# Optimization experiments

Measured on AMD Instinct MI355X. Metric: run time of the kernel, lower is better.

Reference implementation:

```python
import jax, jax.numpy as jnp
import numpy as np

B_SZ, CH, H, W = 32, 256, 28, 28
D_INNER, D_STATE, D_CONV, DT_RANK, DEPTH = 512, 16, 4, 16, 2


def setup_inputs() -> dict:
    key = jax.random.key(0)
    ks = jax.random.split(key, 10)
    s = 0.02
    A = jnp.broadcast_to(jnp.arange(1, D_STATE + 1, dtype=jnp.float32), (DEPTH, D_INNER, D_STATE))
    return {
        "bbox_feats": jax.random.normal(ks[0], (B_SZ, CH, H, W), jnp.float32),
        "norm_w": jnp.ones((DEPTH, CH), jnp.float32),
        "norm_b": jnp.zeros((DEPTH, CH), jnp.float32),
        "in_proj_w": jax.random.normal(ks[1], (DEPTH, 2 * D_INNER, CH), jnp.float32) * s,
        "conv_w": jax.random.normal(ks[2], (DEPTH, D_INNER, D_CONV), jnp.float32) * 0.1,
        "conv_b": jnp.zeros((DEPTH, D_INNER), jnp.float32),
        "x_proj_w": jax.random.normal(ks[3], (DEPTH, DT_RANK + 2 * D_STATE, D_INNER), jnp.float32) * s,
        "dt_proj_w": jax.random.normal(ks[4], (DEPTH, D_INNER, DT_RANK), jnp.float32) * 0.1,
        "dt_proj_b": jax.random.normal(ks[5], (DEPTH, D_INNER), jnp.float32) * 0.1,
        "A_log": jnp.log(A),
        "D_param": jnp.ones((DEPTH, D_INNER), jnp.float32),
        "out_proj_w": jax.random.normal(ks[6], (DEPTH, CH, D_INNER), jnp.float32) * s,
    }


def _layernorm(x, w, b, eps=1e-5):
    mu = jnp.mean(x, axis=-1, keepdims=True)
    var = jnp.mean(jnp.square(x - mu), axis=-1, keepdims=True)
    return (x - mu) * jax.lax.rsqrt(var + eps) * w + b


def _mamba(x, in_w, cw, cb, xp_w, dtp_w, dtp_b, A_log, Dp, out_w):
    # x: [B, L, d_model]
    B, L, _ = x.shape
    xz = jnp.einsum('bld,ed->ble', x, in_w)          # [B, L, 2*d_inner]
    xi, z = jnp.split(xz, 2, axis=-1)                # each [B, L, d_inner]
    # depthwise causal conv1d (kernel D_CONV, left pad D_CONV-1)
    xpad = jnp.pad(xi, ((0, 0), (D_CONV - 1, 0), (0, 0)))
    xc = cb
    for k in range(D_CONV):
        xc = xc + xpad[:, k:k + L, :] * cw[:, k]
    xc = jax.nn.silu(xc)                             # [B, L, d_inner]
    x_dbl = jnp.einsum('bld,ed->ble', xc, xp_w)      # [B, L, dt_rank+2*d_state]
    dt_r = x_dbl[..., :DT_RANK]
    Bm = x_dbl[..., DT_RANK:DT_RANK + D_STATE]
    Cm = x_dbl[..., DT_RANK + D_STATE:]
    dt = jax.nn.softplus(jnp.einsum('blr,dr->bld', dt_r, dtp_w) + dtp_b)  # [B, L, d_inner]
    A = -jnp.exp(A_log)                              # [d_inner, d_state]

    def step(h, inp):
        dt_t, B_t, C_t, x_t = inp                    # [B,d_inner],[B,d_state],[B,d_state],[B,d_inner]
        dA = jnp.exp(dt_t[:, :, None] * A)           # [B, d_inner, d_state]
        h = h * dA + dt_t[:, :, None] * B_t[:, None, :] * x_t[:, :, None]
        y = jnp.einsum('bds,bs->bd', h, C_t)
        return h, y

    h0 = jnp.zeros((B, D_INNER, D_STATE), x.dtype)
    inputs = (jnp.swapaxes(dt, 0, 1), jnp.swapaxes(Bm, 0, 1),
              jnp.swapaxes(Cm, 0, 1), jnp.swapaxes(xc, 0, 1))
    _, ys = jax.lax.scan(step, h0, inputs)
    y = jnp.swapaxes(ys, 0, 1) + xc * Dp             # [B, L, d_inner]
    y = y * jax.nn.silu(z)
    return jnp.einsum('bld,ed->ble', y, out_w)       # [B, L, d_model]


def reference(bbox_feats, norm_w, norm_b, in_proj_w, conv_w, conv_b,
              x_proj_w, dt_proj_w, dt_proj_b, A_log, D_param, out_proj_w):
    B, C, h, w = bbox_feats.shape
    x = bbox_feats
    for i in range(DEPTH):
        xf = jnp.swapaxes(x.reshape(B, C, h * w), -1, -2)   # [B, L, C]
        xn = _layernorm(xf, norm_w[i], norm_b[i])
        ym = _mamba(xn, in_proj_w[i], conv_w[i], conv_b[i], x_proj_w[i],
                    dt_proj_w[i], dt_proj_b[i], A_log[i], D_param[i], out_proj_w[i])
        x = jnp.swapaxes(ym, -1, -2).reshape(B, C, h, w)
    return x
```

## Files before the change

### kernel.cpp

```cpp
#include <hip/hip_runtime.h>
#include <cstdint>
#include <cstddef>

#define BSZ  32
#define CHN  256
#define LSEQ 784
#define DI   512
#define NCH  16

#define PK_TILE  16384
#define PK_NT    7
#define PK_PERB  (PK_NT * PK_TILE)

typedef unsigned short u16;
typedef short s16x8 __attribute__((ext_vector_type(8)));
typedef float f32x4 __attribute__((ext_vector_type(4)));

__device__ __forceinline__ float b2f(u16 u) {
  union { unsigned int i; float f; } v; v.i = ((unsigned int)u) << 16; return v.f;
}
__device__ __forceinline__ u16 f2b(float f) {
  union { float f; unsigned int i; } v; v.f = f;
  unsigned int x = v.i;
  return (u16)((x + 0x7FFFu + ((x >> 16) & 1u)) >> 16);
}

#define SA_HALF(dv, xv, Q0, Q1, Q2, Q3) do {                                  \
  float dx_ = (dv) * (xv);                                                    \
  float w1_ = __expf(-(dv));                                                  \
  float e2_ = w1_*w1_, e4_ = e2_*e2_, e8_ = e4_*e4_;                          \
  float p3_ = e2_*w1_, p5_ = e4_*w1_, p6_ = e4_*e2_, p7_ = p6_*w1_;           \
  float p9_ = e8_*w1_, p10_ = e8_*e2_, p11_ = p10_*w1_, p12_ = e8_*e4_;       \
  float p13_ = p12_*w1_, p14_ = p12_*e2_, p15_ = p14_*w1_, p16_ = e8_*e8_;    \
  h[0]  = h[0]*w1_  + dx_*Q0.x;  h[1]  = h[1]*e2_  + dx_*Q0.y;                \
  h[2]  = h[2]*p3_  + dx_*Q0.z;  h[3]  = h[3]*e4_  + dx_*Q0.w;                \
  h[4]  = h[4]*p5_  + dx_*Q1.x;  h[5]  = h[5]*p6_  + dx_*Q1.y;                \
  h[6]  = h[6]*p7_  + dx_*Q1.z;  h[7]  = h[7]*e8_  + dx_*Q1.w;                \
  h[8]  = h[8]*p9_  + dx_*Q2.x;  h[9]  = h[9]*p10_ + dx_*Q2.y;                \
  h[10] = h[10]*p11_+ dx_*Q2.z;  h[11] = h[11]*p12_+ dx_*Q2.w;                \
  h[12] = h[12]*p13_+ dx_*Q3.x;  h[13] = h[13]*p14_+ dx_*Q3.y;                \
  h[14] = h[14]*p15_+ dx_*Q3.z;  h[15] = h[15]*p16_+ dx_*Q3.w;                \
} while (0)

#define SC_HALF(dv, xv, zv, Q0, Q1, Q2, Q3, R0, R1, R2, R3, YB) do {          \
  SA_HALF(dv, xv, Q0, Q1, Q2, Q3);                                            \
  float ya_ = h[0]*R0.x;  ya_ = fmaf(h[1], R0.y, ya_);                        \
  ya_ = fmaf(h[2], R0.z, ya_);  ya_ = fmaf(h[3], R0.w, ya_);                  \
  float yb_ = h[4]*R1.x;  yb_ = fmaf(h[5], R1.y, yb_);                        \
  yb_ = fmaf(h[6], R1.z, yb_);  yb_ = fmaf(h[7], R1.w, yb_);                  \
  float yc_ = h[8]*R2.x;  yc_ = fmaf(h[9], R2.y, yc_);                        \
  yc_ = fmaf(h[10], R2.z, yc_); yc_ = fmaf(h[11], R2.w, yc_);                 \
  float yd_ = h[12]*R3.x; yd_ = fmaf(h[13], R3.y, yd_);                       \
  yd_ = fmaf(h[14], R3.z, yd_); yd_ = fmaf(h[15], R3.w, yd_);                 \
  float yy_ = (ya_ + yb_) + (yc_ + yd_) + (xv) * dpar;                        \
  float sg_ = (zv) / (1.f + __expf(-(zv)));                                   \
  YB = f2b(yy_ * sg_);                                                        \
} while (0)

__global__ void k_flag(const unsigned* __restrict__ nwraw, int* __restrict__ flag) {
  if (threadIdx.x == 0 && blockIdx.x == 0) {
    flag[0] = (nwraw[0] == 0x3F803F80u) ? 1 : 0;
    flag[1] = 1;
  }
}

struct CanonSrcs { const void* p[11]; };

__global__ __launch_bounds__(256) void k_canon_all(CanonSrcs s,
                                                   u16* __restrict__ ws,
                                                   const int* __restrict__ flag) {
  const int ns[11]  = {512, 512, 524288, 4096, 1024, 49152,
                       16384, 1024, 16384, 1024, 262144};
  const int off[11] = {0, 512, 1024, 525312, 529408, 530432,
                       579584, 595968, 596992, 613376, 614400};
  const int pre[12] = {0, 1, 2, 258, 260, 261, 285, 293, 294, 302, 303, 431};
  int bid = blockIdx.x;
  int seg = 0;
#pragma unroll
  for (int k = 1; k < 11; k++) if (bid >= pre[k]) seg = k;
  int lb = bid - pre[seg];
  int n = ns[seg];
  u16* dst = ws + off[seg];
  int i = lb * 2048 + threadIdx.x;
  if (flag[0]) {
    const u16* src = (const u16*)s.p[seg];
#pragma unroll
    for (int q = 0; q < 8; q++) {
      int j = i + q * 256;
      if (j < n) dst[j] = src[j];
    }
  } else {
    const float* src = (const float*)s.p[seg];
#pragma unroll
    for (int q = 0; q < 8; q++) {
      int j = i + q * 256;
      if (j < n) dst[j] = f2b(src[j]);
    }
  }
}

__global__ __launch_bounds__(256) void k_norm(const void* __restrict__ xv,
                                              int b0,
                                              const int* __restrict__ flag,
                                              const u16* __restrict__ nw,
                                              const u16* __restrict__ nb,
                                              u16* __restrict__ xn) {
  bool isbf = flag[0] != 0;
  int b  = blockIdx.y;
  int gb = b0 + b;
  int l0 = blockIdx.x * 64;
  int tx = threadIdx.x & 63;
  int ty = threadIdx.x >> 6;
  int l  = l0 + tx;
  bool valid = l < LSEQ;
  const u16*   xb16 = (const u16*)xv   + (size_t)gb * CHN * LSEQ;
  const float* xb32 = (const float*)xv + (size_t)gb * CHN * LSEQ;
  float s = 0.f, sq = 0.f;
  for (int c = ty; c < CHN; c += 4) {
    size_t idx = (size_t)c * LSEQ + l;
    float v = 0.f;
    if (valid) v = isbf ? b2f(xb16[idx]) : xb32[idx];
    s += v; sq += v * v;
  }
  __shared__ float rs[4][64], rq[4][64], smu[64], srs[64];
  rs[ty][tx] = s; rq[ty][tx] = sq;
  __syncthreads();
  if (ty == 0) {
    float ss = rs[0][tx] + rs[1][tx] + rs[2][tx] + rs[3][tx];
    float qq = rq[0][tx] + rq[1][tx] + rq[2][tx] + rq[3][tx];
    float mu  = ss * (1.f / CHN);
    float var = qq * (1.f / CHN) - mu * mu;
    smu[tx] = mu;
    srs[tx] = rsqrtf(var + 1e-5f);
  }
  __syncthreads();
  if (valid) {
    float mu = smu[tx], rstd = srs[tx];
    unsigned* Pp = (unsigned*)xn + (size_t)b * PK_PERB
                 + (size_t)(l >> 7) * PK_TILE + (l & 127);
    for (int kp = ty; kp < 128; kp += 4) {
      int c0 = 2 * kp, c1 = c0 + 1;
      size_t i0 = (size_t)c0 * LSEQ + l;
      size_t i1 = (size_t)c1 * LSEQ + l;
      float v0 = isbf ? b2f(xb16[i0]) : xb32[i0];
      float v1 = isbf ? b2f(xb16[i1]) : xb32[i1];
      u16 a0 = f2b((v0 - mu) * rstd * b2f(nw[c0]) + b2f(nb[c0]));
      u16 a1 = f2b((v1 - mu) * rstd * b2f(nw[c1]) + b2f(nb[c1]));
      Pp[(size_t)kp * 128] = (unsigned)a0 | ((unsigned)a1 << 16);
    }
  }
}

template <int MODE>
__global__ __launch_bounds__(256) void k_gmm(const u16* __restrict__ A,
                                             const u16* __restrict__ W,
                                             float* __restrict__ C0,
                                             u16* __restrict__ Cb0,
                                             u16* __restrict__ Cb1,
                                             void* __restrict__ Dout,
                                             const int* __restrict__ flag,
                                             int b0, int K, int Ntot) {
  __shared__ unsigned ldsA[128 * 20];
  __shared__ unsigned ldsW[64 * 20];
  int tid = threadIdx.x;
  int m0 = blockIdx.x * 128;
  int n0 = blockIdx.y * 64;
  int b  = blockIdx.z;
  int w    = tid >> 6;
  int l15  = tid & 15;
  int quad = (tid >> 4) & 3;
  int kp = tid & 15;
  int mo = tid >> 4;
  int wn = tid >> 2;
  int wc = tid & 3;

  f32x4 acc[8];
#pragma unroll
  for (int i = 0; i < 8; i++)
#pragma unroll
    for (int r = 0; r < 4; r++) acc[i][r] = 0.f;

  for (int k0 = 0; k0 < K; k0 += 32) {
    __syncthreads();
    if constexpr (MODE == 1) {
      int mo2 = tid & 15;
      int kpp = tid >> 4;
      const unsigned* Pb = (const unsigned*)A + (size_t)b * PK_PERB
                         + (size_t)blockIdx.x * PK_TILE
                         + (size_t)((k0 >> 1) + kpp) * 128 + mo2 * 8;
      int4 r0 = *(const int4*)Pb;
      int4 r1 = *(const int4*)(Pb + 4);
      unsigned vals[8] = {(unsigned)r0.x, (unsigned)r0.y, (unsigned)r0.z, (unsigned)r0.w,
                          (unsigned)r1.x, (unsigned)r1.y, (unsigned)r1.z, (unsigned)r1.w};
#pragma unroll
      for (int q = 0; q < 8; q++)
        ldsA[(mo2 * 8 + q) * 20 + kpp] = vals[q];
    } else {
      const u16* Ab = A + (size_t)b * K * LSEQ;
      int mg = m0 + mo * 8;
      unsigned lo[4] = {0u, 0u, 0u, 0u}, hi[4] = {0u, 0u, 0u, 0u};
      if (mg < LSEQ) {
        int4 r0 = *(const int4*)(Ab + (size_t)(k0 + 2 * kp) * LSEQ + mg);
        int4 r1 = *(const int4*)(Ab + (size_t)(k0 + 2 * kp + 1) * LSEQ + mg);
        lo[0] = (unsigned)r0.x; lo[1] = (unsigned)r0.y;
        lo[2] = (unsigned)r0.z; lo[3] = (unsigned)r0.w;
        hi[0] = (unsigned)r1.x; hi[1] = (unsigned)r1.y;
        hi[2] = (unsigned)r1.z; hi[3] = (unsigned)r1.w;
      }
#pragma unroll
      for (int j = 0; j < 8; j++) {
        unsigned lov = (lo[j >> 1] >> ((j & 1) * 16)) & 0xFFFFu;
        unsigned hiv = (hi[j >> 1] >> ((j & 1) * 16)) & 0xFFFFu;
        ldsA[(mo * 8 + j) * 20 + kp] = lov | (hiv << 16);
      }
    }
    {
      int ng = n0 + wn;
      int4 r = make_int4(0, 0, 0, 0);
      if (ng < Ntot) r = *(const int4*)(W + (size_t)ng * K + k0 + wc * 8);
      *(int4*)(ldsW + wn * 20 + wc * 4) = r;
    }
    __syncthreads();
    s16x8 bf = *(const s16x8*)(ldsW + ((w * 16 + l15) * 20 + quad * 4));
#pragma unroll
    for (int mi = 0; mi < 8; mi++) {
      s16x8 af = *(const s16x8*)(ldsA + ((mi * 16 + l15) * 20 + quad * 4));
      acc[mi] = __builtin_amdgcn_mfma_f32_16x16x32_bf16(af, bf, acc[mi], 0, 0, 0);
    }
  }

  int n_g = n0 + w * 16 + l15;
  if (n_g >= Ntot) return;
#pragma unroll
  for (int mi = 0; mi < 8; mi++) {
    int mb = m0 + mi * 16;
    if (mb >= LSEQ) break;
    int m = mb + quad * 4;
    float v0 = acc[mi][0], v1 = acc[mi][1], v2 = acc[mi][2], v3 = acc[mi][3];
    if constexpr (MODE == 0) {
      if (n_g < 16) {
        float* crow = C0 + ((size_t)b * Ntot + n_g) * LSEQ + m;
        *(float4*)crow = make_float4(v0, v1, v2, v3);
      } else {
        float* bcf = (float*)Dout;
        size_t rbase = ((size_t)b * LSEQ + m) * 32 + (n_g - 16);
        bcf[rbase]      = v0;
        bcf[rbase + 32] = v1;
        bcf[rbase + 64] = v2;
        bcf[rbase + 96] = v3;
      }
    } else if constexpr (MODE == 3) {
      size_t off = ((size_t)(b0 + b) * Ntot + n_g) * LSEQ + m;
      if (flag[0]) {
        u16* crow = (u16*)Dout + off;
        ((unsigned*)crow)[0] = (unsigned)f2b(v0) | ((unsigned)f2b(v1) << 16);
        ((unsigned*)crow)[1] = (unsigned)f2b(v2) | ((unsigned)f2b(v3) << 16);
      } else {
        float* crow = (float*)Dout + off;
        *(float4*)crow = make_float4(v0, v1, v2, v3);
      }
    } else {
      u16* crow;
      if constexpr (MODE == 1) {
        crow = (n_g < DI) ? (Cb0 + ((size_t)b * DI + n_g) * LSEQ + m)
                          : (Cb1 + ((size_t)b * DI + (n_g - DI)) * LSEQ + m);
      } else {
        crow = Cb0 + ((size_t)b * Ntot + n_g) * LSEQ + m;
      }
      ((unsigned*)crow)[0] = (unsigned)f2b(v0) | ((unsigned)f2b(v1) << 16);
      ((unsigned*)crow)[1] = (unsigned)f2b(v2) | ((unsigned)f2b(v3) << 16);
    }
  }
}

__global__ __launch_bounds__(256) void k_conv(const u16* __restrict__ xi,
                                              const u16* __restrict__ cw,
                                              const u16* __restrict__ cb,
                                              u16* __restrict__ xc) {
  int b = blockIdx.z, e = blockIdx.y;
  int l = blockIdx.x * 256 + threadIdx.x;
  if (l >= LSEQ) return;
  const u16* xr = xi + ((size_t)b * DI + e) * LSEQ;
  float acc = b2f(cb[e]);
#pragma unroll
  for (int k = 0; k < 4; k++) {
    int li = l - 3 + k;
    if (li >= 0) acc += b2f(xr[li]) * b2f(cw[e * 4 + k]);
  }
  acc = acc / (1.f + __expf(-acc));
  xc[((size_t)b * DI + e) * LSEQ + l] = f2b(acc);
}

__device__ __forceinline__ float softplus_f(float x) {
  float t = __expf(x);
  return (x > 20.f) ? x : __logf(1.f + t);
}

__global__ __launch_bounds__(256) void k_dtp(const float* __restrict__ xd,
                                             const u16* __restrict__ dtw,
                                             const u16* __restrict__ dtbv,
                                             u16* __restrict__ dtp) {
  __shared__ float Ls[16][64];
  int b  = blockIdx.y;
  int l0 = blockIdx.x * 64;
  int tid = threadIdx.x;
  const float* xb = xd + (size_t)b * 48 * LSEQ;
  for (int idx = tid; idx < 16 * 64; idx += 256) {
    int r = idx >> 6, lo = idx & 63;
    int l = l0 + lo;
    Ls[r][lo] = (l < LSEQ) ? xb[(size_t)r * LSEQ + l] : 0.f;
  }
  __syncthreads();
  int tx = tid & 63, ty = tid >> 6;
  int l = l0 + tx;
  if (l >= LSEQ) return;
  u16* drow = dtp + (size_t)b * DI * LSEQ + l;
  for (int eg = 0; eg < 128; eg++) {
    int e = ty * 128 + eg;
    float acc = b2f(dtbv[e]);
#pragma unroll
    for (int r = 0; r < 16; r++) acc += Ls[r][tx] * b2f(dtw[e * 16 + r]);
    drow[(size_t)e * LSEQ] = f2b(softplus_f(acc));
  }
}

__global__ __launch_bounds__(256, 2) void k_scanA(const u16* __restrict__ dtp,
                                                  const float* __restrict__ BC,
                                                  const u16* __restrict__ xc,
                                                  const u16* __restrict__ A_log,
                                                  float* __restrict__ Sb,
                                                  float* __restrict__ hloc) {
  __shared__ unsigned xs[256 * 13];
  __shared__ unsigned ds[256 * 13];
  __shared__ float bcsA[26 * 4 * 16];
  int tid = threadIdx.x;
  int b = blockIdx.x >> 5;
  int r = blockIdx.x & 31;
  int e     = ((r >> 2) << 6) + (tid & 63);
  int cq    = r & 3;
  int w     = tid >> 6;
  int chunk = cq * 4 + w;
  bool pow_ok = true;
#pragma unroll
  for (int n = 0; n < 16; n++) {
    float an = -__expf(b2f(A_log[e * 16 + n]));
    pow_ok = pow_ok && (fabsf(an + (float)(n + 1)) < 0.02f * (n + 1));
  }
  float h[16];
#pragma unroll
  for (int n = 0; n < 16; n++) h[n] = 0.f;
  float S = 0.f;
  int lbase = chunk * 50;
  const unsigned* gx = (const unsigned*)(xc  + ((size_t)b * DI + e) * LSEQ + lbase);
  const unsigned* gd = (const unsigned*)(dtp + ((size_t)b * DI + e) * LSEQ + lbase);
  unsigned* myx = xs + tid * 13;
  unsigned* myd = ds + tid * 13;
  float a[16];
  if (!pow_ok) {
#pragma unroll
    for (int n = 0; n < 16; n++) a[n] = -__expf(b2f(A_log[e * 16 + n]));
  }
#pragma unroll
  for (int t = 0; t < 2; t++) {
    int nd = (t == 0) ? 13 : ((chunk == 15) ? 4 : 12);
    const unsigned* gxo = gx + t * 13;
    const unsigned* gdo = gd + t * 13;
    for (int j = 0; j < nd; j++) { myx[j] = gxo[j]; myd[j] = gdo[j]; }
    int NS = (t == 0) ? 26 : 24;
    int total = NS * 64;
    for (int k = 0; k < 7; k++) {
      int lin = tid + k * 256;
      if (lin < total) {
        int q = lin & 15;
        int rest = lin >> 4;
        int wc = rest & 3;
        int s = rest >> 2;
        int l = (cq * 4 + wc) * 50 + t * 26 + s;
        bcsA[lin] = BC[((size_t)b * LSEQ + l) * 32 + q];
      }
    }
    __syncthreads();
    if (pow_ok) {
      for (int j = 0; j < nd; j++) {
        unsigned wd = myd[j], wx = myx[j];
        float d0 = b2f((u16)(wd & 0xFFFFu)), x0 = b2f((u16)(wx & 0xFFFFu));
        float d1 = b2f((u16)(wd >> 16)),     x1 = b2f((u16)(wx >> 16));
        const float4* bp0 = (const float4*)(bcsA + (((2 * j) * 4 + w) << 4));
        float4 P0 = bp0[0], P1 = bp0[1], P2 = bp0[2], P3 = bp0[3];
        const float4* bp1 = (const float4*)(bcsA + (((2 * j + 1) * 4 + w) << 4));
        float4 Q0 = bp1[0], Q1 = bp1[1], Q2 = bp1[2], Q3 = bp1[3];
        S += d0;
        SA_HALF(d0, x0, P0, P1, P2, P3);
        S += d1;
        SA_HALF(d1, x1, Q0, Q1, Q2, Q3);
      }
    } else {
      for (int j = 0; j < nd; j++) {
        unsigned wd = myd[j], wx = myx[j];
        for (int hs = 0; hs < 2; hs++) {
          float d  = b2f((u16)(hs ? (wd >> 16) : (wd & 0xFFFFu)));
          float xt = b2f((u16)(hs ? (wx >> 16) : (wx & 0xFFFFu)));
          S += d;
          const float4* bp = (const float4*)(bcsA + (((2 * j + hs) * 4 + w) << 4));
          float4 B0 = bp[0], B1 = bp[1], B2 = bp[2], B3 = bp[3];
          float Bv[16] = {B0.x,B0.y,B0.z,B0.w, B1.x,B1.y,B1.z,B1.w,
                          B2.x,B2.y,B2.z,B2.w, B3.x,B3.y,B3.z,B3.w};
          float dx = d * xt;
#pragma unroll
          for (int n = 0; n < 16; n++) {
            float da = __expf(d * a[n]);
            h[n] = h[n] * da + dx * Bv[n];
          }
        }
      }
    }
    __syncthreads();
  }
  Sb[((size_t)b * DI + e) * NCH + chunk] = S;
  size_t base = (((size_t)b * DI + e) * NCH + chunk) * 16;
  float4* Hp = (float4*)(hloc + base);
#pragma unroll
  for (int q = 0; q < 4; q++)
    Hp[q] = make_float4(h[q*4], h[q*4+1], h[q*4+2], h[q*4+3]);
}

__global__ __launch_bounds__(256) void k_comb(const u16* __restrict__ A_log,
                                              const float* __restrict__ Sb,
                                              float* hloc) {
  int idx = blockIdx.x * 256 + threadIdx.x;
  int n  = idx & 15;
  int be = idx >> 4;
  int e  = be & (DI - 1);
  float an = -__expf(b2f(A_log[e * 16 + n]));
  size_t hbase = (size_t)be * (NCH * 16) + n;
  size_t sbase = (size_t)be * NCH;
  float h = 0.f;
#pragma unroll
  for (int c = 0; c < NCH; c++) {
    size_t o = hbase + (size_t)c * 16;
    float hl = hloc[o];
    float p  = __expf(an * Sb[sbase + c]);
    hloc[o] = h;
    h = hl + p * h;
  }
}

__global__ __launch_bounds__(256, 2) void k_scanC(const u16* __restrict__ dtp,
                                                  const float* __restrict__ BC,
                                                  const u16* __restrict__ zp,
                                                  const u16* __restrict__ A_log,
                                                  const u16* __restrict__ Dp,
                                                  const float* __restrict__ hinit,
                                                  u16* xcy) {
  __shared__ unsigned xs[256 * 13];
  __shared__ unsigned zs[256 * 13];
  __shared__ unsigned ds[256 * 13];
  __shared__ float bcsC[26 * 4 * 32];
  int tid = threadIdx.x;
  int b = blockIdx.x >> 5;
  int r = blockIdx.x & 31;
  int e     = ((r >> 2) << 6) + (tid & 63);
  int cq    = r & 3;
  int w     = tid >> 6;
  int chunk = cq * 4 + w;
  bool pow_ok = true;
#pragma unroll
  for (int n = 0; n < 16; n++) {
    float an = -__expf(b2f(A_log[e * 16 + n]));
    pow_ok = pow_ok && (fabsf(an + (float)(n + 1)) < 0.02f * (n + 1));
  }
  float h[16];
  {
    size_t base = (((size_t)b * DI + e) * NCH + chunk) * 16;
    const float4* Hp = (const float4*)(hinit + base);
#pragma unroll
    for (int q = 0; q < 4; q++) {
      float4 v = Hp[q];
      h[q*4] = v.x; h[q*4+1] = v.y; h[q*4+2] = v.z; h[q*4+3] = v.w;
    }
  }
  float dpar = b2f(Dp[e]);
  int lbase = chunk * 50;
  unsigned* gy        = (unsigned*)(xcy + ((size_t)b * DI + e) * LSEQ + lbase);
  const unsigned* gz  = (const unsigned*)(zp  + ((size_t)b * DI + e) * LSEQ + lbase);
  const unsigned* gd  = (const unsigned*)(dtp + ((size_t)b * DI + e) * LSEQ + lbase);
  unsigned* myx = xs + tid * 13;
  unsigned* myz = zs + tid * 13;
  unsigned* myd = ds + tid * 13;
  float a[16];
  if (!pow_ok) {
#pragma unroll
    for (int n = 0; n < 16; n++) a[n] = -__expf(b2f(A_log[e * 16 + n]));
  }
#pragma unroll
  for (int t = 0; t < 2; t++) {
    int nd = (t == 0) ? 13 : ((chunk == 15) ? 4 : 12);
    const unsigned* gxo = gy + t * 13;
    const unsigned* gzo = gz + t * 13;
    const unsigned* gdo = gd + t * 13;
    for (int j = 0; j < nd; j++) {
      myx[j] = gxo[j]; myz[j] = gzo[j]; myd[j] = gdo[j];
    }
    int NS = (t == 0) ? 26 : 24;
    int total = NS * 128;
    for (int k = 0; k < 13; k++) {
      int lin = tid + k * 256;
      if (lin < total) {
        int q = lin & 31;
        int rest = lin >> 5;
        int wc = rest & 3;
        int s = rest >> 2;
        int l = (cq * 4 + wc) * 50 + t * 26 + s;
        bcsC[lin] = BC[((size_t)b * LSEQ + l) * 32 + q];
      }
    }
    __syncthreads();
    unsigned* gyo = gy + t * 13;
    if (pow_ok) {
      for (int j = 0; j < nd; j++) {
        unsigned wd = myd[j], wx = myx[j], wz = myz[j];
        float d0 = b2f((u16)(wd & 0xFFFFu)), x0 = b2f((u16)(wx & 0xFFFFu)),
              z0 = b2f((u16)(wz & 0xFFFFu));
        float d1 = b2f((u16)(wd >> 16)),     x1 = b2f((u16)(wx >> 16)),
              z1 = b2f((u16)(wz >> 16));
        const float4* bp0 = (const float4*)(bcsC + (((2 * j) * 4 + w) << 5));
        float4 P0 = bp0[0], P1 = bp0[1], P2 = bp0[2], P3 = bp0[3];
        float4 R0 = bp0[4], R1 = bp0[5], R2 = bp0[6], R3 = bp0[7];
        const float4* bp1 = (const float4*)(bcsC + (((2 * j + 1) * 4 + w) << 5));
        float4 Q0 = bp1[0], Q1 = bp1[1], Q2 = bp1[2], Q3 = bp1[3];
        float4 T0 = bp1[4], T1 = bp1[5], T2 = bp1[6], T3 = bp1[7];
        u16 y0, y1;
        SC_HALF(d0, x0, z0, P0, P1, P2, P3, R0, R1, R2, R3, y0);
        SC_HALF(d1, x1, z1, Q0, Q1, Q2, Q3, T0, T1, T2, T3, y1);
        myx[j] = (unsigned)y0 | ((unsigned)y1 << 16);
      }
    } else {
      for (int j = 0; j < nd; j++) {
        unsigned wd = myd[j], wx = myx[j], wz = myz[j];
        unsigned ypk = 0u;
        for (int hs = 0; hs < 2; hs++) {
          float d  = b2f((u16)(hs ? (wd >> 16) : (wd & 0xFFFFu)));
          float xt = b2f((u16)(hs ? (wx >> 16) : (wx & 0xFFFFu)));
          float z  = b2f((u16)(hs ? (wz >> 16) : (wz & 0xFFFFu)));
          const float4* bp = (const float4*)(bcsC + (((2 * j + hs) * 4 + w) << 5));
          float4 B0 = bp[0], B1 = bp[1], B2 = bp[2], B3 = bp[3];
          float4 C0 = bp[4], C1 = bp[5], C2 = bp[6], C3 = bp[7];
          float Bv[16] = {B0.x,B0.y,B0.z,B0.w, B1.x,B1.y,B1.z,B1.w,
                          B2.x,B2.y,B2.z,B2.w, B3.x,B3.y,B3.z,B3.w};
          float Cv[16] = {C0.x,C0.y,C0.z,C0.w, C1.x,C1.y,C1.z,C1.w,
                          C2.x,C2.y,C2.z,C2.w, C3.x,C3.y,C3.z,C3.w};
          float dx = d * xt;
          float yacc = 0.f;
#pragma unroll
          for (int n = 0; n < 16; n++) {
            float da = __expf(d * a[n]);
            h[n] = h[n] * da + dx * Bv[n];
            yacc += h[n] * Cv[n];
          }
          float yy = yacc + xt * dpar;
          float sg = 1.f / (1.f + __expf(-z));
          u16 yb = f2b(yy * (z * sg));
          ypk |= ((unsigned)yb) << (16 * hs);
        }
        myx[j] = ypk;
      }
    }
    for (int j = 0; j < nd; j++) gyo[j] = myx[j];
    __syncthreads();
  }
}

extern "C" void kernel_launch(void* const* d_in, const int* in_sizes, int n_in,
                              void* d_out, int out_size, void* d_ws, size_t ws_size,
                              hipStream_t stream) {
  u16* ws = (u16*)d_ws;

  u16* c_nw  = ws;
  u16* c_nb  = ws + 512;
  u16* c_inw = ws + 1024;
  u16* c_cw  = ws + 525312;
  u16* c_cb  = ws + 529408;
  u16* c_xpw = ws + 530432;
  u16* c_dtw = ws + 579584;
  u16* c_dtb = ws + 595968;
  u16* c_al  = ws + 596992;
  u16* c_dp  = ws + 613376;
  u16* c_ow  = ws + 614400;
  int* flag  = (int*)(ws + 876544);
  const size_t WREG = 876552;

  k_flag<<<1, 64, 0, stream>>>((const unsigned*)d_in[1], flag);
  {
    CanonSrcs s;
    for (int k = 0; k < 11; k++) s.p[k] = d_in[k + 1];
    k_canon_all<<<431, 256, 0, stream>>>(s, ws, flag);
  }

  size_t fixed_bytes = WREG * 2;
  size_t per_batch   = 4ull * DI * LSEQ * 2;
  int Bg = 1;
  for (int g = 32; g >= 1; g >>= 1) {
    if (ws_size >= fixed_bytes + (size_t)g * per_batch) { Bg = g; break; }
  }

  size_t plane = (size_t)Bg * DI * LSEQ;
  u16*   pb = ws + WREG;
  u16*   xi = pb;
  float* fb = (float*)pb;
  float* bc = fb;
  float* xd = bc + (size_t)Bg * LSEQ * 32;
  float* Sb = xd;
  float* hl = Sb + (size_t)Bg * DI * NCH;
  u16*   zp = pb + plane;
  u16*   xc = pb + 2 * plane;
  u16*   dtx1 = pb + 3 * plane;
  u16*   dtp = dtx1;
  u16*   x1  = dtx1;
  u16*   xn = xc;

  for (int b0 = 0; b0 < BSZ; b0 += Bg) {
    for (int i = 0; i < 2; i++) {
      if (i == 0)
        k_norm<<<dim3(13, Bg), 256, 0, stream>>>(
            d_in[0], b0, flag, c_nw, c_nb, xn);
      else
        k_norm<<<dim3(13, Bg), 256, 0, stream>>>(
            (const void*)x1, 0, flag + 1, c_nw + CHN, c_nb + CHN, xn);
      k_gmm<1><<<dim3(7, 16, Bg), 256, 0, stream>>>(
          xn, c_inw + (size_t)i * 1024 * CHN, nullptr, xi, zp,
          nullptr, nullptr, 0, CHN, 1024);
      k_conv<<<dim3(4, 512, Bg), 256, 0, stream>>>(
          xi, c_cw + i * DI * 4, c_cb + i * DI, xc);
      k_gmm<0><<<dim3(7, 1, Bg), 256, 0, stream>>>(
          xc, c_xpw + (size_t)i * 48 * DI, xd, nullptr, nullptr,
          (void*)bc, nullptr, 0, DI, 48);
      k_dtp<<<dim3(13, Bg), 256, 0, stream>>>(
          xd, c_dtw + i * DI * 16, c_dtb + i * DI, dtp);
      k_scanA<<<Bg * 32, 256, 0, stream>>>(
          dtp, bc, xc, c_al + i * DI * 16, Sb, hl);
      k_comb<<<Bg * 32, 256, 0, stream>>>(c_al + i * DI * 16, Sb, hl);
      k_scanC<<<Bg * 32, 256, 0, stream>>>(
          dtp, bc, zp, c_al + i * DI * 16, c_dp + i * DI, hl, xc);
      if (i == 0)
        k_gmm<2><<<dim3(7, 4, Bg), 256, 0, stream>>>(
            xc, c_ow, nullptr, x1, nullptr,
            nullptr, nullptr, 0, DI, CHN);
      else
        k_gmm<3><<<dim3(7, 4, Bg), 256, 0, stream>>>(
            xc, c_ow + (size_t)CHN * DI, nullptr, nullptr, nullptr,
            d_out, flag, b0, DI, CHN);
    }
  }
}
```

Before: 894.2 us.

## Drop packed-tile layernorm output and unroll scan loops over fixed chunk length

The layernorm kernel now writes its normalized bf16 output in the plain channel-major layout instead of the pre-packed K-pair tile layout, and the GEMM's MODE 1 path reuses the generic strided loader. The selective-scan inner loops in both scan phases now run a compile-time-bounded, fully unrolled trip count and zero-fill entries past the real length, so per-step register arrays can stay in registers. This trades the coalesced packed GEMM A-load for simpler layernorm stores and adds a little redundant work in the padded scan iterations.

```diff
diff --git a/kernel.cpp b/kernel.cpp
--- a/kernel.cpp
+++ b/kernel.cpp
@@ -7,10 +7,6 @@
 #define LSEQ 784
 #define DI   512
 #define NCH  16
-
-#define PK_TILE  16384
-#define PK_NT    7
-#define PK_PERB  (PK_NT * PK_TILE)
 
 typedef unsigned short u16;
 typedef short s16x8 __attribute__((ext_vector_type(8)));
@@ -136,17 +132,11 @@
   __syncthreads();
   if (valid) {
     float mu = smu[tx], rstd = srs[tx];
-    unsigned* Pp = (unsigned*)xn + (size_t)b * PK_PERB
-                 + (size_t)(l >> 7) * PK_TILE + (l & 127);
-    for (int kp = ty; kp < 128; kp += 4) {
-      int c0 = 2 * kp, c1 = c0 + 1;
-      size_t i0 = (size_t)c0 * LSEQ + l;
-      size_t i1 = (size_t)c1 * LSEQ + l;
-      float v0 = isbf ? b2f(xb16[i0]) : xb32[i0];
-      float v1 = isbf ? b2f(xb16[i1]) : xb32[i1];
-      u16 a0 = f2b((v0 - mu) * rstd * b2f(nw[c0]) + b2f(nb[c0]));
-      u16 a1 = f2b((v1 - mu) * rstd * b2f(nw[c1]) + b2f(nb[c1]));
-      Pp[(size_t)kp * 128] = (unsigned)a0 | ((unsigned)a1 << 16);
+    u16* xnb = xn + (size_t)b * CHN * LSEQ;
+    for (int c = ty; c < CHN; c += 4) {
+      size_t idx = (size_t)c * LSEQ + l;
+      float v = isbf ? b2f(xb16[idx]) : xb32[idx];
+      xnb[idx] = f2b((v - mu) * rstd * b2f(nw[c]) + b2f(nb[c]));
     }
   }
 }
@@ -174,6 +164,8 @@
   int wn = tid >> 2;
   int wc = tid & 3;
 
+  const u16* Ab = A + (size_t)b * K * LSEQ;
+
   f32x4 acc[8];
 #pragma unroll
   for (int i = 0; i < 8; i++)
@@ -182,21 +174,7 @@
 
   for (int k0 = 0; k0 < K; k0 += 32) {
     __syncthreads();
-    if constexpr (MODE == 1) {
-      int mo2 = tid & 15;
-      int kpp = tid >> 4;
-      const unsigned* Pb = (const unsigned*)A + (size_t)b * PK_PERB
-                         + (size_t)blockIdx.x * PK_TILE
-                         + (size_t)((k0 >> 1) + kpp) * 128 + mo2 * 8;
-      int4 r0 = *(const int4*)Pb;
-      int4 r1 = *(const int4*)(Pb + 4);
-      unsigned vals[8] = {(unsigned)r0.x, (unsigned)r0.y, (unsigned)r0.z, (unsigned)r0.w,
-                          (unsigned)r1.x, (unsigned)r1.y, (unsigned)r1.z, (unsigned)r1.w};
-#pragma unroll
-      for (int q = 0; q < 8; q++)
-        ldsA[(mo2 * 8 + q) * 20 + kpp] = vals[q];
-    } else {
-      const u16* Ab = A + (size_t)b * K * LSEQ;
+    {
       int mg = m0 + mo * 8;
       unsigned lo[4] = {0u, 0u, 0u, 0u}, hi[4] = {0u, 0u, 0u, 0u};
       if (mg < LSEQ) {
@@ -381,8 +359,11 @@
     }
     __syncthreads();
     if (pow_ok) {
-      for (int j = 0; j < nd; j++) {
-        unsigned wd = myd[j], wx = myx[j];
+      const int NDT = (t == 0) ? 13 : 12;
+#pragma unroll
+      for (int j = 0; j < NDT; j++) {
+        unsigned wd = (j < nd) ? myd[j] : 0u;
+        unsigned wx = (j < nd) ? myx[j] : 0u;
         float d0 = b2f((u16)(wd & 0xFFFFu)), x0 = b2f((u16)(wx & 0xFFFFu));
         float d1 = b2f((u16)(wd >> 16)),     x1 = b2f((u16)(wx >> 16));
         const float4* bp0 = (const float4*)(bcsA + (((2 * j) * 4 + w) << 4));
@@ -517,8 +498,12 @@
     __syncthreads();
     unsigned* gyo = gy + t * 13;
     if (pow_ok) {
-      for (int j = 0; j < nd; j++) {
-        unsigned wd = myd[j], wx = myx[j], wz = myz[j];
+      const int NDT = (t == 0) ? 13 : 12;
+#pragma unroll
+      for (int j = 0; j < NDT; j++) {
+        unsigned wd = (j < nd) ? myd[j] : 0u;
+        unsigned wx = (j < nd) ? myx[j] : 0u;
+        unsigned wz = (j < nd) ? myz[j] : 0u;
         float d0 = b2f((u16)(wd & 0xFFFFu)), x0 = b2f((u16)(wx & 0xFFFFu)),
               z0 = b2f((u16)(wz & 0xFFFFu));
         float d1 = b2f((u16)(wd >> 16)),     x1 = b2f((u16)(wx >> 16)),
```

After: 995.7 us. 11.4% more time.
